# Optimization experiments

Hardware: AMD Instinct MI355X
Metric: run time of the kernel (lower is better)

## Reference

```python
import jax, jax.numpy as jnp
import numpy as np

B, N, MAX_DEG = 256, 512, 6
F_IN, H = 62, 128  # layers = [62, 128, 128]
NUM_DEG = MAX_DEG + 1  # degree buckets 0..6


def gather_neighbors(atoms, edges, maskvalue):
    # atoms [B,N,F], edges [B,N,D] with -1 padding -> [B,N,D,F]
    idx = jnp.maximum(edges, 0)
    neigh = jax.vmap(lambda a, e: a[e])(atoms, idx)
    return jnp.where(edges[..., None] < 0, jnp.asarray(maskvalue, atoms.dtype), neigh)


def nfp_conv(atoms, edges, W, b):
    # W [NUM_DEG, F_in, F_out], b [NUM_DEG, F_out]
    deg = jnp.sum(edges >= 0, axis=-1)  # [B,N]
    neigh = gather_neighbors(atoms, edges, 0.0)
    summed = neigh.sum(axis=2) + atoms  # include self, [B,N,F_in]
    out = jnp.zeros(summed.shape[:2] + (W.shape[-1],), summed.dtype)
    for d in range(NUM_DEG):  # small fixed set of degree buckets
        h = jax.nn.sigmoid(summed @ W[d] + b[d])
        out = out + h * (deg == d)[..., None].astype(h.dtype)
    return out


def graph_pool(atoms, edges):
    # max over self + neighbors
    neigh = gather_neighbors(atoms, edges, -jnp.inf)
    allf = jnp.concatenate([atoms[:, :, None, :], neigh], axis=2)  # [B,N,D+1,F]
    return allf.max(axis=2)


def setup_inputs() -> dict:
    key = jax.random.key(0)
    ka, ke, km, k0, k1, k2, k3 = jax.random.split(key, 7)
    a = jax.random.normal(ka, (B, N, F_IN), dtype=jnp.float32)
    e = jax.random.randint(ke, (B, N, MAX_DEG), 0, N, dtype=jnp.int32)
    # introduce -1 padding so atoms have varied degrees 0..6
    u = jax.random.uniform(km, (B, N, MAX_DEG))
    e = jnp.where(u < 0.6, e, -1).astype(jnp.int32)
    W0 = jax.random.normal(k0, (NUM_DEG, F_IN, H), dtype=jnp.float32) * 0.1
    b0 = jax.random.normal(k1, (NUM_DEG, H), dtype=jnp.float32) * 0.1
    W1 = jax.random.normal(k2, (NUM_DEG, H, H), dtype=jnp.float32) * 0.1
    b1 = jax.random.normal(k3, (NUM_DEG, H), dtype=jnp.float32) * 0.1
    return {"a": a, "e": e, "W0": W0, "b0": b0, "W1": W1, "b1": b1}


def reference(a, e, W0, b0, W1, b1):
    x = nfp_conv(a, e, W0, b0)
    x = graph_pool(x, e)
    x = nfp_conv(x, e, W1, b1)
    x = graph_pool(x, e)
    return x.sum(axis=1)  # SubgraphSum: [B, H]
```

## Files before the change

### kernel.cpp

```cpp
#include <hip/hip_runtime.h>
#include <math.h>

#define BB 256
#define NN 512
#define DD 6
#define F_IN 62
#define HH 128
#define ND 7
#define TOTAL (BB*NN)

typedef __bf16 bf16x8 __attribute__((ext_vector_type(8)));
typedef float f32x4 __attribute__((ext_vector_type(4)));

__device__ __forceinline__ unsigned short f2bf(float f) {
    unsigned u = __builtin_bit_cast(unsigned, f);
    u = (u + 0x7FFFu + ((u >> 16) & 1u)) >> 16;
    return (unsigned short)u;
}
__device__ __forceinline__ float lo2f(unsigned x) { return __builtin_bit_cast(float, x << 16); }
__device__ __forceinline__ float hi2f(unsigned x) { return __builtin_bit_cast(float, x & 0xFFFF0000u); }


__global__ __launch_bounds__(512) void k_sort_batch(const int* __restrict__ e,
                                                    int* __restrict__ deg,
                                                    int* __restrict__ order) {
    __shared__ unsigned int lh[ND];
    __shared__ unsigned int base[ND];
    const int b = blockIdx.x;
    const int t = threadIdx.x;
    if (t < ND) lh[t] = 0u;
    __syncthreads();
    const int u = b * NN + t;
    int d = 0;
#pragma unroll
    for (int j = 0; j < DD; ++j) d += (e[u * DD + j] >= 0) ? 1 : 0;
    deg[u] = d;
    unsigned int r = atomicAdd(&lh[d], 1u);
    __syncthreads();
    if (t == 0) {
        unsigned int acc = 0;
        for (int k = 0; k < ND; ++k) { base[k] = acc; acc += lh[k]; }
    }
    __syncthreads();
    order[b * NN + base[d] + r] = u;
}


__global__ __launch_bounds__(256) void k_prep_a(const float* __restrict__ a,
                                                unsigned short* __restrict__ Ap) {
    int u = blockIdx.x * 256 + threadIdx.x;
    int r = u >> 3;
    int c0 = (u & 7) * 8;
    unsigned short h[8];
#pragma unroll
    for (int i = 0; i < 8; ++i) {
        int c = c0 + i;
        h[i] = (c < F_IN) ? f2bf(a[(size_t)r * F_IN + c]) : (unsigned short)0;
    }
    uint4 p;
    p.x = (unsigned)h[0] | ((unsigned)h[1] << 16);
    p.y = (unsigned)h[2] | ((unsigned)h[3] << 16);
    p.z = (unsigned)h[4] | ((unsigned)h[5] << 16);
    p.w = (unsigned)h[6] | ((unsigned)h[7] << 16);
    *(uint4*)&Ap[(size_t)r * 64 + c0] = p;
}


__global__ void k_prep_wt(const float* __restrict__ W, unsigned short* __restrict__ WT,
                          int F, int K) {
    int n = blockIdx.x;
    int d = blockIdx.y;
    for (int k = threadIdx.x; k < K; k += 64) {
        float v = (k < F) ? W[((size_t)d * F + k) * HH + n] : 0.f;
        WT[((size_t)d * HH + n) * K + k] = f2bf(v);
    }
}


template<int KB>
__global__ __launch_bounds__(256, 3)
void k_conv_mfma(const unsigned short* __restrict__ Xp,
                 const int* __restrict__ e,
                 const unsigned short* __restrict__ WT,
                 const float* __restrict__ bias,
                 const int* __restrict__ order,
                 const int* __restrict__ deg,
                 unsigned short* __restrict__ Y) {
    constexpr int K = KB * 8;
    constexpr int LOGKB = (KB == 16) ? 4 : 3;
    __shared__ unsigned short sP[64 * 128];
    __shared__ int vT[64];
    __shared__ int degT[64];
    __shared__ int eT[64 * DD];

    const int t = threadIdx.x;
    const int l = t & 63;
    const int w = t >> 6;

    const int bi = blockIdx.x;
    const int x8 = bi & 7;
    const int j = bi >> 3;
    const int batch = x8 + 8 * (j >> 3);
    const int tile = j & 7;
    const int g0 = batch * NN + tile * 64;

    if (t < 64) {
        int v = order[g0 + t];
        vT[t] = v;
        degT[t] = deg[v];
    }
    __syncthreads();
    for (int i = t; i < 64 * DD; i += 256) eT[i] = e[vT[i / DD] * DD + (i % DD)];
    __syncthreads();

    for (int u = t; u < 64 * KB; u += 256) {
        const int kb = u & (KB - 1);
        const int n = u >> LOGKB;
        const int v = vT[n];
        const int nbase = v & ~(NN - 1);
        float s[8];
        {
            uint4 p = *(const uint4*)(Xp + (size_t)v * K + kb * 8);
            s[0] = lo2f(p.x); s[1] = hi2f(p.x); s[2] = lo2f(p.y); s[3] = hi2f(p.y);
            s[4] = lo2f(p.z); s[5] = hi2f(p.z); s[6] = lo2f(p.w); s[7] = hi2f(p.w);
        }
#pragma unroll
        for (int jj = 0; jj < DD; ++jj) {
            int idx = eT[n * DD + jj];
            if (idx >= 0) {
                uint4 p = *(const uint4*)(Xp + (size_t)(nbase + idx) * K + kb * 8);
                s[0] += lo2f(p.x); s[1] += hi2f(p.x); s[2] += lo2f(p.y); s[3] += hi2f(p.y);
                s[4] += lo2f(p.z); s[5] += hi2f(p.z); s[6] += lo2f(p.w); s[7] += hi2f(p.w);
            }
        }
        uint4 r;
        r.x = (unsigned)f2bf(s[0]) | ((unsigned)f2bf(s[1]) << 16);
        r.y = (unsigned)f2bf(s[2]) | ((unsigned)f2bf(s[3]) << 16);
        r.z = (unsigned)f2bf(s[4]) | ((unsigned)f2bf(s[5]) << 16);
        r.w = (unsigned)f2bf(s[6]) | ((unsigned)f2bf(s[7]) << 16);
        const int kbs = kb ^ (n & 7);
        *(uint4*)&sP[(n * KB + kbs) * 8] = r;
    }
    __syncthreads();

    const int dlo = degT[0];
    const int dhi = degT[63];
    const int lr = l & 15;
    const int lq = l >> 4;

    for (int d = dlo; d <= dhi; ++d) {
        bf16x8 bf[K / 32][2];
#pragma unroll
        for (int kk = 0; kk < K / 32; ++kk)
#pragma unroll
            for (int nb = 0; nb < 2; ++nb) {
                int ncol = w * 32 + nb * 16 + lr;
                int krow = kk * 32 + lq * 8;
                bf[kk][nb] = *(const bf16x8*)(WT + ((size_t)d * HH + ncol) * K + krow);
            }

        f32x4 acc[4][2];
#pragma unroll
        for (int mb = 0; mb < 4; ++mb)
#pragma unroll
            for (int nb = 0; nb < 2; ++nb) {
                f32x4 z = {0.f, 0.f, 0.f, 0.f};
                acc[mb][nb] = z;
            }

#pragma unroll
        for (int kk = 0; kk < K / 32; ++kk) {
#pragma unroll
            for (int mb = 0; mb < 4; ++mb) {
                int nrow = mb * 16 + lr;
                int kbp = kk * 4 + lq;
                int kbs = kbp ^ (nrow & 7);
                bf16x8 af = *(const bf16x8*)&sP[(nrow * KB + kbs) * 8];
                acc[mb][0] = __builtin_amdgcn_mfma_f32_16x16x32_bf16(af, bf[kk][0], acc[mb][0], 0, 0, 0);
                acc[mb][1] = __builtin_amdgcn_mfma_f32_16x16x32_bf16(af, bf[kk][1], acc[mb][1], 0, 0, 0);
            }
        }

        if (dlo == dhi) {
            __syncthreads();
#pragma unroll
            for (int mb = 0; mb < 4; ++mb)
#pragma unroll
                for (int nb = 0; nb < 2; ++nb) {
                    int col = w * 32 + nb * 16 + lr;
                    float bv = bias[d * HH + col];
#pragma unroll
                    for (int r = 0; r < 4; ++r) {
                        int n = mb * 16 + lq * 4 + r;
                        float z = 1.f / (1.f + __expf(-(acc[mb][nb][r] + bv)));
                        sP[n * HH + col] = f2bf(z);
                    }
                }
            __syncthreads();
            for (int u = t; u < 64 * HH / 8; u += 256) {
                int n = u >> 4;
                int c8 = (u & 15) * 8;
                uint4 p = *(const uint4*)&sP[n * HH + c8];
                *(uint4*)&Y[(size_t)vT[n] * HH + c8] = p;
            }
        } else {
#pragma unroll
            for (int mb = 0; mb < 4; ++mb)
#pragma unroll
                for (int nb = 0; nb < 2; ++nb) {
                    int col = w * 32 + nb * 16 + lr;
                    float bv = bias[d * HH + col];
#pragma unroll
                    for (int r = 0; r < 4; ++r) {
                        int n = mb * 16 + lq * 4 + r;
                        if (degT[n] == d) {
                            float z = 1.f / (1.f + __expf(-(acc[mb][nb][r] + bv)));
                            Y[(size_t)vT[n] * HH + col] = f2bf(z);
                        }
                    }
                }
        }
    }
}


__global__ __launch_bounds__(256) void k_pool_bf(const unsigned short* __restrict__ X,
                                                 const int* __restrict__ e,
                                                 unsigned short* __restrict__ P) {
    const int t = threadIdx.x;
    const int bi = blockIdx.x;
    const int x8 = bi & 7;
    const int j = bi >> 3;
    const int batch = x8 + 8 * (j >> 5);
    const int sub = j & 31;
    const int u = batch * NN + sub * 16 + (t >> 4);
    const int c8 = (t & 15) * 8;
    const int nbase = u & ~(NN - 1);
    float m[8];
    {
        uint4 p = *(const uint4*)(X + (size_t)u * HH + c8);
        m[0] = lo2f(p.x); m[1] = hi2f(p.x); m[2] = lo2f(p.y); m[3] = hi2f(p.y);
        m[4] = lo2f(p.z); m[5] = hi2f(p.z); m[6] = lo2f(p.w); m[7] = hi2f(p.w);
    }
#pragma unroll
    for (int jj = 0; jj < DD; ++jj) {
        int idx = e[u * DD + jj];
        if (idx >= 0) {
            uint4 p = *(const uint4*)(X + (size_t)(nbase + idx) * HH + c8);
            m[0] = fmaxf(m[0], lo2f(p.x)); m[1] = fmaxf(m[1], hi2f(p.x));
            m[2] = fmaxf(m[2], lo2f(p.y)); m[3] = fmaxf(m[3], hi2f(p.y));
            m[4] = fmaxf(m[4], lo2f(p.z)); m[5] = fmaxf(m[5], hi2f(p.z));
            m[6] = fmaxf(m[6], lo2f(p.w)); m[7] = fmaxf(m[7], hi2f(p.w));
        }
    }
    uint4 r;
    r.x = (unsigned)f2bf(m[0]) | ((unsigned)f2bf(m[1]) << 16);
    r.y = (unsigned)f2bf(m[2]) | ((unsigned)f2bf(m[3]) << 16);
    r.z = (unsigned)f2bf(m[4]) | ((unsigned)f2bf(m[5]) << 16);
    r.w = (unsigned)f2bf(m[6]) | ((unsigned)f2bf(m[7]) << 16);
    *(uint4*)&P[(size_t)u * HH + c8] = r;
}


__global__ __launch_bounds__(256) void k_pool_sum_part(const unsigned short* __restrict__ X,
                                                       const int* __restrict__ e,
                                                       float* __restrict__ partial) {
    __shared__ float red[16][HH + 4];
    const int t = threadIdx.x;
    const int bi = blockIdx.x;
    const int x8 = bi & 7;
    const int j = bi >> 3;
    const int b = x8 + 8 * (j >> 3);
    const int chunk = j & 7;
    const int slot = t >> 4;
    const int c8 = (t & 15) * 8;
    float acc[8];
#pragma unroll
    for (int i = 0; i < 8; ++i) acc[i] = 0.f;

    for (int n = chunk * 64 + slot; n < chunk * 64 + 64; n += 16) {
        int u = b * NN + n;
        float m[8];
        uint4 p = *(const uint4*)(X + (size_t)u * HH + c8);
        m[0] = lo2f(p.x); m[1] = hi2f(p.x); m[2] = lo2f(p.y); m[3] = hi2f(p.y);
        m[4] = lo2f(p.z); m[5] = hi2f(p.z); m[6] = lo2f(p.w); m[7] = hi2f(p.w);
#pragma unroll
        for (int jj = 0; jj < DD; ++jj) {
            int idx = e[u * DD + jj];
            if (idx >= 0) {
                uint4 q = *(const uint4*)(X + (size_t)(b * NN + idx) * HH + c8);
                m[0] = fmaxf(m[0], lo2f(q.x)); m[1] = fmaxf(m[1], hi2f(q.x));
                m[2] = fmaxf(m[2], lo2f(q.y)); m[3] = fmaxf(m[3], hi2f(q.y));
                m[4] = fmaxf(m[4], lo2f(q.z)); m[5] = fmaxf(m[5], hi2f(q.z));
                m[6] = fmaxf(m[6], lo2f(q.w)); m[7] = fmaxf(m[7], hi2f(q.w));
            }
        }
#pragma unroll
        for (int i = 0; i < 8; ++i) acc[i] += m[i];
    }
#pragma unroll
    for (int i = 0; i < 8; ++i) red[slot][c8 + i] = acc[i];
    __syncthreads();
    if (t < HH) {
        float s = 0.f;
#pragma unroll
        for (int k = 0; k < 16; ++k) s += red[k][t];
        partial[(size_t)(b * 8 + chunk) * HH + t] = s;
    }
}


__global__ __launch_bounds__(256) void k_sum_final(const float* __restrict__ partial,
                                                   float* __restrict__ out) {
    int g = blockIdx.x * 256 + threadIdx.x;
    int b = g >> 7;
    int c = g & 127;
    float s = 0.f;
#pragma unroll
    for (int k = 0; k < 8; ++k) s += partial[(size_t)(b * 8 + k) * HH + c];
    out[g] = s;
}


extern "C" void kernel_launch(void* const* d_in, const int* in_sizes, int n_in,
                              void* d_out, int out_size, void* d_ws, size_t ws_size,
                              hipStream_t stream) {
    const float* a  = (const float*)d_in[0];
    const int*   e  = (const int*)d_in[1];
    const float* W0 = (const float*)d_in[2];
    const float* b0 = (const float*)d_in[3];
    const float* W1 = (const float*)d_in[4];
    const float* b1 = (const float*)d_in[5];
    float* out = (float*)d_out;

    char* ws = (char*)d_ws;
    const size_t XB = (size_t)TOTAL * HH * 2;
    unsigned short* xbuf = (unsigned short*)ws;
    unsigned short* pbuf = (unsigned short*)(ws + XB);
    unsigned short* Ap   = (unsigned short*)(ws + 2 * XB);
    float* partial = (float*)Ap;
    unsigned short* WT0  = (unsigned short*)(ws + 2 * XB + (size_t)TOTAL * 64 * 2);
    unsigned short* WT1  = WT0 + (size_t)ND * HH * 64;
    char* ip = (char*)(WT1 + (size_t)ND * HH * 128);
    int* deg   = (int*)ip;
    int* order = (int*)(ip + (size_t)TOTAL * 4);

    hipLaunchKernelGGL(k_sort_batch, dim3(BB), dim3(NN), 0, stream, e, deg, order);

    hipLaunchKernelGGL(k_prep_a, dim3(TOTAL * 8 / 256), dim3(256), 0, stream, a, Ap);
    hipLaunchKernelGGL(k_prep_wt, dim3(HH, ND), dim3(64), 0, stream, W0, WT0, F_IN, 64);
    hipLaunchKernelGGL(k_prep_wt, dim3(HH, ND), dim3(64), 0, stream, W1, WT1, HH, 128);

    hipLaunchKernelGGL((k_conv_mfma<8>),  dim3(TOTAL / 64), dim3(256), 0, stream,
                       Ap, e, WT0, b0, order, deg, xbuf);
    hipLaunchKernelGGL(k_pool_bf, dim3(TOTAL / 16), dim3(256), 0, stream, xbuf, e, pbuf);
    hipLaunchKernelGGL((k_conv_mfma<16>), dim3(TOTAL / 64), dim3(256), 0, stream,
                       pbuf, e, WT1, b1, order, deg, xbuf);
    hipLaunchKernelGGL(k_pool_sum_part, dim3(BB * 8), dim3(256), 0, stream, xbuf, e, partial);
    hipLaunchKernelGGL(k_sum_final, dim3(BB * HH / 256), dim3(256), 0, stream, partial, out);
}
```

Before: 163.4 us.

## Pad degree buckets to 16-row groups so each MFMA block uses one weight set

The degree sort now pads each degree bucket to a multiple of 16 rows and records a per-16-row-group degree plus a tile count per batch. The conv kernel then runs exactly one weight matrix per 16-row MFMA sub-block, instead of looping over every degree present in a 64-row tile and masking the scattered stores. This removes the redundant GEMM passes on mixed-degree tiles and always uses the coalesced LDS-staged store. The cost is padding rows, extra launched blocks that exit early, and an extra init pass over the order array.

Result: faster. 146.5 us (-10.4%).

```diff
diff --git a/kernel.cpp b/kernel.cpp
--- a/kernel.cpp
+++ b/kernel.cpp
@@ -8,6 +8,9 @@
 #define HH 128
 #define ND 7
 #define TOTAL (BB*NN)
+#define OPB 640
+#define GPB 40
+#define TPB 10
 
 typedef __bf16 bf16x8 __attribute__((ext_vector_type(8)));
 typedef float f32x4 __attribute__((ext_vector_type(4)));
@@ -21,28 +24,34 @@
 __device__ __forceinline__ float hi2f(unsigned x) { return __builtin_bit_cast(float, x & 0xFFFF0000u); }
 
 
-__global__ __launch_bounds__(512) void k_sort_batch(const int* __restrict__ e,
-                                                    int* __restrict__ deg,
-                                                    int* __restrict__ order) {
-    __shared__ unsigned int lh[ND];
-    __shared__ unsigned int base[ND];
+__global__ __launch_bounds__(512) void k_sort16(const int* __restrict__ e,
+                                                int* __restrict__ order,
+                                                int* __restrict__ dgrp,
+                                                int* __restrict__ ntiles) {
+    __shared__ unsigned int scnt[ND];
+    __shared__ unsigned int sbase[ND + 1];
     const int b = blockIdx.x;
     const int t = threadIdx.x;
-    if (t < ND) lh[t] = 0u;
-    __syncthreads();
-    const int u = b * NN + t;
+    if (t < ND) scnt[t] = 0u;
+    for (int i = t; i < OPB; i += 512) order[b * OPB + i] = -1;
+    __syncthreads();
     int d = 0;
 #pragma unroll
-    for (int j = 0; j < DD; ++j) d += (e[u * DD + j] >= 0) ? 1 : 0;
-    deg[u] = d;
-    unsigned int r = atomicAdd(&lh[d], 1u);
+    for (int j = 0; j < DD; ++j) d += (e[(b * NN + t) * DD + j] >= 0) ? 1 : 0;
+    unsigned rk = atomicAdd(&scnt[d], 1u);
     __syncthreads();
     if (t == 0) {
-        unsigned int acc = 0;
-        for (int k = 0; k < ND; ++k) { base[k] = acc; acc += lh[k]; }
-    }
-    __syncthreads();
-    order[b * NN + base[d] + r] = u;
+        unsigned acc = 0;
+        for (int k = 0; k < ND; ++k) { sbase[k] = acc; acc += (scnt[k] + 15u) & ~15u; }
+        sbase[ND] = acc;
+        for (int k = 0; k < ND; ++k)
+            for (unsigned g = sbase[k] >> 4; g < (sbase[k + 1] >> 4); ++g)
+                dgrp[b * GPB + g] = k;
+        for (unsigned g = acc >> 4; g < GPB; ++g) dgrp[b * GPB + g] = 0;
+        ntiles[b] = (int)((acc + 63u) >> 6);
+    }
+    __syncthreads();
+    order[b * OPB + sbase[d] + rk] = t;
 }
 
 
@@ -84,13 +93,13 @@
                  const unsigned short* __restrict__ WT,
                  const float* __restrict__ bias,
                  const int* __restrict__ order,
-                 const int* __restrict__ deg,
+                 const int* __restrict__ dgrp,
+                 const int* __restrict__ ntiles,
                  unsigned short* __restrict__ Y) {
     constexpr int K = KB * 8;
     constexpr int LOGKB = (KB == 16) ? 4 : 3;
     __shared__ unsigned short sP[64 * 128];
     __shared__ int vT[64];
-    __shared__ int degT[64];
     __shared__ int eT[64 * DD];
 
     const int t = threadIdx.x;
@@ -100,37 +109,36 @@
     const int bi = blockIdx.x;
     const int x8 = bi & 7;
     const int j = bi >> 3;
-    const int batch = x8 + 8 * (j >> 3);
-    const int tile = j & 7;
-    const int g0 = batch * NN + tile * 64;
-
-    if (t < 64) {
-        int v = order[g0 + t];
-        vT[t] = v;
-        degT[t] = deg[v];
-    }
-    __syncthreads();
-    for (int i = t; i < 64 * DD; i += 256) eT[i] = e[vT[i / DD] * DD + (i % DD)];
+    const int batch = x8 + 8 * (j / TPB);
+    const int tile = j % TPB;
+    if (tile >= ntiles[batch]) return;
+
+    if (t < 64) vT[t] = order[batch * OPB + tile * 64 + t];
+    __syncthreads();
+    for (int i = t; i < 64 * DD; i += 256) {
+        int v = vT[i / DD];
+        if (v >= 0) eT[i] = e[((size_t)batch * NN + v) * DD + (i % DD)];
+    }
     __syncthreads();
 
     for (int u = t; u < 64 * KB; u += 256) {
         const int kb = u & (KB - 1);
         const int n = u >> LOGKB;
         const int v = vT[n];
-        const int nbase = v & ~(NN - 1);
-        float s[8];
-        {
-            uint4 p = *(const uint4*)(Xp + (size_t)v * K + kb * 8);
+        float s[8] = {0.f, 0.f, 0.f, 0.f, 0.f, 0.f, 0.f, 0.f};
+        if (v >= 0) {
+            const unsigned short* base = Xp + (size_t)batch * NN * K;
+            uint4 p = *(const uint4*)(base + (size_t)v * K + kb * 8);
             s[0] = lo2f(p.x); s[1] = hi2f(p.x); s[2] = lo2f(p.y); s[3] = hi2f(p.y);
             s[4] = lo2f(p.z); s[5] = hi2f(p.z); s[6] = lo2f(p.w); s[7] = hi2f(p.w);
-        }
-#pragma unroll
-        for (int jj = 0; jj < DD; ++jj) {
-            int idx = eT[n * DD + jj];
-            if (idx >= 0) {
-                uint4 p = *(const uint4*)(Xp + (size_t)(nbase + idx) * K + kb * 8);
-                s[0] += lo2f(p.x); s[1] += hi2f(p.x); s[2] += lo2f(p.y); s[3] += hi2f(p.y);
-                s[4] += lo2f(p.z); s[5] += hi2f(p.z); s[6] += lo2f(p.w); s[7] += hi2f(p.w);
+#pragma unroll
+            for (int jj = 0; jj < DD; ++jj) {
+                int idx = eT[n * DD + jj];
+                if (idx >= 0) {
+                    uint4 q = *(const uint4*)(base + (size_t)idx * K + kb * 8);
+                    s[0] += lo2f(q.x); s[1] += hi2f(q.x); s[2] += lo2f(q.y); s[3] += hi2f(q.y);
+                    s[4] += lo2f(q.z); s[5] += hi2f(q.z); s[6] += lo2f(q.w); s[7] += hi2f(q.w);
+                }
             }
         }
         uint4 r;
@@ -143,82 +151,69 @@
     }
     __syncthreads();
 
-    const int dlo = degT[0];
-    const int dhi = degT[63];
     const int lr = l & 15;
     const int lq = l >> 4;
 
-    for (int d = dlo; d <= dhi; ++d) {
-        bf16x8 bf[K / 32][2];
-#pragma unroll
-        for (int kk = 0; kk < K / 32; ++kk)
-#pragma unroll
-            for (int nb = 0; nb < 2; ++nb) {
-                int ncol = w * 32 + nb * 16 + lr;
-                int krow = kk * 32 + lq * 8;
-                bf[kk][nb] = *(const bf16x8*)(WT + ((size_t)d * HH + ncol) * K + krow);
+    int dg[4];
+#pragma unroll
+    for (int mb = 0; mb < 4; ++mb) dg[mb] = dgrp[batch * GPB + tile * 4 + mb];
+
+    bf16x8 bf[K / 32][2];
+    f32x4 acc[4][2];
+    int dprev = -1;
+#pragma unroll
+    for (int mb = 0; mb < 4; ++mb) {
+        const int d = dg[mb];
+        if (d != dprev) {
+#pragma unroll
+            for (int kk = 0; kk < K / 32; ++kk)
+#pragma unroll
+                for (int nb = 0; nb < 2; ++nb) {
+                    int ncol = w * 32 + nb * 16 + lr;
+                    int krow = kk * 32 + lq * 8;
+                    bf[kk][nb] = *(const bf16x8*)(WT + ((size_t)d * HH + ncol) * K + krow);
+                }
+            dprev = d;
+        }
+        f32x4 z0 = {0.f, 0.f, 0.f, 0.f};
+        f32x4 z1 = {0.f, 0.f, 0.f, 0.f};
+        const int nrow = mb * 16 + lr;
+#pragma unroll
+        for (int kk = 0; kk < K / 32; ++kk) {
+            int kbp = kk * 4 + lq;
+            int kbs = kbp ^ (nrow & 7);
+            bf16x8 af = *(const bf16x8*)&sP[(nrow * KB + kbs) * 8];
+            z0 = __builtin_amdgcn_mfma_f32_16x16x32_bf16(af, bf[kk][0], z0, 0, 0, 0);
+            z1 = __builtin_amdgcn_mfma_f32_16x16x32_bf16(af, bf[kk][1], z1, 0, 0, 0);
+        }
+        acc[mb][0] = z0;
+        acc[mb][1] = z1;
+    }
+
+    __syncthreads();
+#pragma unroll
+    for (int mb = 0; mb < 4; ++mb) {
+        const int d = dg[mb];
+#pragma unroll
+        for (int nb = 0; nb < 2; ++nb) {
+            int col = w * 32 + nb * 16 + lr;
+            float bv = bias[d * HH + col];
+#pragma unroll
+            for (int r = 0; r < 4; ++r) {
+                int n = mb * 16 + lq * 4 + r;
+                float z = 1.f / (1.f + __expf(-(acc[mb][nb][r] + bv)));
+                sP[n * HH + col] = f2bf(z);
             }
-
-        f32x4 acc[4][2];
-#pragma unroll
-        for (int mb = 0; mb < 4; ++mb)
-#pragma unroll
-            for (int nb = 0; nb < 2; ++nb) {
-                f32x4 z = {0.f, 0.f, 0.f, 0.f};
-                acc[mb][nb] = z;
-            }
-
-#pragma unroll
-        for (int kk = 0; kk < K / 32; ++kk) {
-#pragma unroll
-            for (int mb = 0; mb < 4; ++mb) {
-                int nrow = mb * 16 + lr;
-                int kbp = kk * 4 + lq;
-                int kbs = kbp ^ (nrow & 7);
-                bf16x8 af = *(const bf16x8*)&sP[(nrow * KB + kbs) * 8];
-                acc[mb][0] = __builtin_amdgcn_mfma_f32_16x16x32_bf16(af, bf[kk][0], acc[mb][0], 0, 0, 0);
-                acc[mb][1] = __builtin_amdgcn_mfma_f32_16x16x32_bf16(af, bf[kk][1], acc[mb][1], 0, 0, 0);
-            }
-        }
-
-        if (dlo == dhi) {
-            __syncthreads();
-#pragma unroll
-            for (int mb = 0; mb < 4; ++mb)
-#pragma unroll
-                for (int nb = 0; nb < 2; ++nb) {
-                    int col = w * 32 + nb * 16 + lr;
-                    float bv = bias[d * HH + col];
-#pragma unroll
-                    for (int r = 0; r < 4; ++r) {
-                        int n = mb * 16 + lq * 4 + r;
-                        float z = 1.f / (1.f + __expf(-(acc[mb][nb][r] + bv)));
-                        sP[n * HH + col] = f2bf(z);
-                    }
-                }
-            __syncthreads();
-            for (int u = t; u < 64 * HH / 8; u += 256) {
-                int n = u >> 4;
-                int c8 = (u & 15) * 8;
-                uint4 p = *(const uint4*)&sP[n * HH + c8];
-                *(uint4*)&Y[(size_t)vT[n] * HH + c8] = p;
-            }
-        } else {
-#pragma unroll
-            for (int mb = 0; mb < 4; ++mb)
-#pragma unroll
-                for (int nb = 0; nb < 2; ++nb) {
-                    int col = w * 32 + nb * 16 + lr;
-                    float bv = bias[d * HH + col];
-#pragma unroll
-                    for (int r = 0; r < 4; ++r) {
-                        int n = mb * 16 + lq * 4 + r;
-                        if (degT[n] == d) {
-                            float z = 1.f / (1.f + __expf(-(acc[mb][nb][r] + bv)));
-                            Y[(size_t)vT[n] * HH + col] = f2bf(z);
-                        }
-                    }
-                }
+        }
+    }
+    __syncthreads();
+    for (int u = t; u < 1024; u += 256) {
+        int n = u >> 4;
+        int c8 = (u & 15) * 8;
+        int v = vT[n];
+        if (v >= 0) {
+            uint4 p = *(const uint4*)&sP[n * HH + c8];
+            *(uint4*)&Y[((size_t)batch * NN + v) * HH + c8] = p;
         }
     }
 }
@@ -342,20 +337,21 @@
     unsigned short* WT0  = (unsigned short*)(ws + 2 * XB + (size_t)TOTAL * 64 * 2);
     unsigned short* WT1  = WT0 + (size_t)ND * HH * 64;
     char* ip = (char*)(WT1 + (size_t)ND * HH * 128);
-    int* deg   = (int*)ip;
-    int* order = (int*)(ip + (size_t)TOTAL * 4);
-
-    hipLaunchKernelGGL(k_sort_batch, dim3(BB), dim3(NN), 0, stream, e, deg, order);
+    int* order  = (int*)ip;
+    int* dgrp   = (int*)(ip + (size_t)BB * OPB * 4);
+    int* ntiles = (int*)(ip + (size_t)BB * (OPB + GPB) * 4);
+
+    hipLaunchKernelGGL(k_sort16, dim3(BB), dim3(NN), 0, stream, e, order, dgrp, ntiles);
 
     hipLaunchKernelGGL(k_prep_a, dim3(TOTAL * 8 / 256), dim3(256), 0, stream, a, Ap);
     hipLaunchKernelGGL(k_prep_wt, dim3(HH, ND), dim3(64), 0, stream, W0, WT0, F_IN, 64);
-    hipLaunchKernelGGL(k_prep_wt, dim3(HH, ND), dim3(64), 0, stream, W1, WT1, HH, 128);
-
-    hipLaunchKernelGGL((k_conv_mfma<8>),  dim3(TOTAL / 64), dim3(256), 0, stream,
-                       Ap, e, WT0, b0, order, deg, xbuf);
+    hipLaunchKernelGGL(k_prep_wt, dim3(HH, ND), dim3(64), 0, stream, W1, WT1, HH, HH);
+
+    hipLaunchKernelGGL((k_conv_mfma<8>),  dim3(BB * TPB), dim3(256), 0, stream,
+                       Ap, e, WT0, b0, order, dgrp, ntiles, xbuf);
     hipLaunchKernelGGL(k_pool_bf, dim3(TOTAL / 16), dim3(256), 0, stream, xbuf, e, pbuf);
-    hipLaunchKernelGGL((k_conv_mfma<16>), dim3(TOTAL / 64), dim3(256), 0, stream,
-                       pbuf, e, WT1, b1, order, deg, xbuf);
+    hipLaunchKernelGGL((k_conv_mfma<16>), dim3(BB * TPB), dim3(256), 0, stream,
+                       pbuf, e, WT1, b1, order, dgrp, ntiles, xbuf);
     hipLaunchKernelGGL(k_pool_sum_part, dim3(BB * 8), dim3(256), 0, stream, xbuf, e, partial);
     hipLaunchKernelGGL(k_sum_final, dim3(BB * HH / 256), dim3(256), 0, stream, partial, out);
 }
```
